# Performance work log

Measured on AMD Instinct MI355X. Metric: run time of the kernel, lower is better.

Reference implementation:

```python
import jax, jax.numpy as jnp
import numpy as np

NUM_CLUSTERS = 10
NUM_ITERS = 20
RTOL, ATOL = 1e-5, 1e-6  # torch.allclose defaults with atol=1e-6 as in source


def _kmeans(tokens, valid, key):
    """Weighted k-means equivalent to kmeans_fast over the valid subset.

    tokens: [n, d] float; valid: [n] bool. Invalid tokens get zero weight in the
    per-cluster means, which is mathematically identical to removing them
    (as the torch code does via boolean indexing) while keeping static shapes.
    """
    n, d = tokens.shape
    # init centroids = random choice of NUM_CLUSTERS valid tokens (torch uses randperm)
    r = jax.random.uniform(key, (n,))
    init_idx = jnp.argsort(jnp.where(valid, r, 2.0))[:NUM_CLUSTERS]
    centroids0 = tokens[init_idx]  # [K, d]
    w = valid.astype(tokens.dtype)  # [n]
    tok_sq = jnp.sum(tokens * tokens, axis=1)  # [n]

    def step(carry, _):
        c, done = carry
        # squared euclidean distances [n, K] via expansion (same math as sum((t-c)^2))
        d2 = tok_sq[:, None] - 2.0 * (tokens @ c.T) + jnp.sum(c * c, axis=1)[None, :]
        labels = jnp.argmin(d2, axis=1)  # [n]
        onehot = jax.nn.one_hot(labels, NUM_CLUSTERS, dtype=tokens.dtype) * w[:, None]
        counts = onehot.sum(axis=0)              # [K]
        sums = onehot.T @ tokens                 # [K, d]
        new_c = jnp.where(counts[:, None] > 0, sums / jnp.maximum(counts, 1.0)[:, None], c)
        conv = jnp.all(jnp.abs(c - new_c) <= ATOL + RTOL * jnp.abs(new_c))
        # torch breaks BEFORE assigning, so on convergence the OLD centroids are kept
        c_next = jnp.where(done | conv, c, new_c)
        return (c_next, done | conv), None

    (c, _), _ = jax.lax.scan(step, (centroids0, jnp.array(False)), None, length=NUM_ITERS)
    return c


def setup_inputs() -> dict:
    key = jax.random.key(0)
    kx, km = jax.random.split(key)
    x = jax.random.normal(kx, (1, 2048, 160, 160), dtype=jnp.float32)
    mask = jax.random.uniform(km, (1, 1, 160, 160), dtype=jnp.float32)
    return {"x": x, "mask": mask}


def reference(x, mask):
    # x: [1, C, H, W]; mask: [1, 1, H, W] (already matching spatial size)
    mb = (mask > 0).astype(mask.dtype)
    mb = jnp.transpose(mb, (1, 0, 2, 3))          # [1, 1, H, W]
    mask_emb = x * mb                              # [1, C, H, W]
    valid = jnp.any(mask_emb != 0, axis=(0, 1))    # [H, W]
    _, C, H, W = x.shape
    tokens = mask_emb[0].reshape(C, H * W).T       # [HW, C]
    valid = valid.reshape(-1)                      # [HW]
    # n_valid > 10 by construction -> kmeans branch (as in source for real masks)
    centroids = _kmeans(tokens, valid, jax.random.key(42))
    return centroids  # [10, C]
```

## Files before the change

### kernel.cpp

```cpp
#include <hip/hip_runtime.h>
#include <stdint.h>

#define HW 25600
#define C  2048
#define K  10
#define NITER 20
#define RTOL_ 1e-5f
#define ATOL_ 1e-6f
#define NCH 16
#define CCH (C / NCH)

__device__ __align__(4) unsigned char g_valid[HW];
__device__ __align__(4) unsigned char g_labels[HW];
__device__ float g_tok_sq[HW];
__device__ float g_r[HW];
__device__ __align__(16) float  g_cent[K * C];
__device__ __align__(16) double g_cent64[K * C];
__device__ float g_csq[K];
__device__ int   g_counts[K];
__device__ unsigned g_done;
__device__ double g_part[NCH * K * HW];
__device__ double g_spart[2 * K * C];
__device__ double g_psq[8 * HW];
__device__ __align__(4) unsigned char g_pany[8 * HW];

__global__ __launch_bounds__(256) void prepA_kernel(const float* __restrict__ X,
                                                    const float* __restrict__ mask) {
    const int chunk = blockIdx.x & 7;
    const int hw0 = (blockIdx.x >> 3) * 1024 + threadIdx.x * 4;
    const float4 m4 = *(const float4*)(mask + hw0);
    const float mb0 = (m4.x > 0.0f) ? 1.0f : 0.0f;
    const float mb1 = (m4.y > 0.0f) ? 1.0f : 0.0f;
    const float mb2 = (m4.z > 0.0f) ? 1.0f : 0.0f;
    const float mb3 = (m4.w > 0.0f) ? 1.0f : 0.0f;
    const float* xp = X + hw0 + (size_t)(chunk * 256) * HW;
    double a0 = 0.0, a1 = 0.0, a2 = 0.0, a3 = 0.0;
    int n0 = 0, n1 = 0, n2 = 0, n3 = 0;
    for (int cc = 0; cc < 256; ++cc) {
        const float4 x = *(const float4*)(xp + (size_t)cc * HW);
        float v0 = x.x * mb0, v1 = x.y * mb1, v2 = x.z * mb2, v3 = x.w * mb3;
        n0 |= (v0 != 0.0f); n1 |= (v1 != 0.0f);
        n2 |= (v2 != 0.0f); n3 |= (v3 != 0.0f);
        a0 = fma((double)v0, (double)v0, a0);
        a1 = fma((double)v1, (double)v1, a1);
        a2 = fma((double)v2, (double)v2, a2);
        a3 = fma((double)v3, (double)v3, a3);
    }
    double* ps = g_psq + chunk * HW + hw0;
    ps[0] = a0; ps[1] = a1; ps[2] = a2; ps[3] = a3;
    *(uchar4*)&g_pany[chunk * HW + hw0] =
        make_uchar4((unsigned char)n0, (unsigned char)n1,
                    (unsigned char)n2, (unsigned char)n3);
}

__device__ __forceinline__ uint32_t rotl32(uint32_t v, int d) {
    return (v << d) | (v >> (32 - d));
}

__global__ __launch_bounds__(256) void rng_kernel() {
    const int hw = blockIdx.x * 256 + threadIdx.x;
    double s0 = (g_psq[0 * HW + hw] + g_psq[1 * HW + hw]) +
                (g_psq[2 * HW + hw] + g_psq[3 * HW + hw]);
    double s1 = (g_psq[4 * HW + hw] + g_psq[5 * HW + hw]) +
                (g_psq[6 * HW + hw] + g_psq[7 * HW + hw]);
    g_tok_sq[hw] = (float)(s0 + s1);
    int any = 0;
#pragma unroll
    for (int j = 0; j < 8; ++j) any |= g_pany[j * HW + hw];
    g_valid[hw] = any ? 1 : 0;

    const uint32_t k0 = 0u, k1 = 42u;
    uint32_t ks[3] = {k0, k1, k0 ^ k1 ^ 0x1BD11BDAu};
    uint32_t x0 = 0u + ks[0];
    uint32_t x1 = (uint32_t)hw + ks[1];
    const int rot[2][4] = {{13, 15, 26, 6}, {17, 29, 16, 24}};
#pragma unroll
    for (int g = 0; g < 5; ++g) {
#pragma unroll
        for (int j = 0; j < 4; ++j) {
            x0 += x1;
            x1 = rotl32(x1, rot[g & 1][j]);
            x1 ^= x0;
        }
        x0 += ks[(g + 1) % 3];
        x1 += ks[(g + 2) % 3] + (uint32_t)(g + 1);
    }
    uint32_t bits = x0 ^ x1;
    float u = __uint_as_float((bits >> 9) | 0x3f800000u) - 1.0f;
    g_r[hw] = any ? u : 2.0f;
}

__global__ __launch_bounds__(1024) void select_kernel(const float* __restrict__ X,
                                                      const float* __restrict__ mask) {
    __shared__ unsigned long long wmin[16];
    __shared__ unsigned long long bcast;
    __shared__ int sh_idx[K];
    const int tid = threadIdx.x;
    const int lane = tid & 63, wv = tid >> 6;
    unsigned long long key[25];
#pragma unroll
    for (int j = 0; j < 25; ++j) {
        const int i = j * 1024 + tid;
        key[j] = ((unsigned long long)__float_as_uint(g_r[i]) << 32) | (unsigned)i;
    }
    for (int round = 0; round < K; ++round) {
        unsigned long long best = ~0ull;
#pragma unroll
        for (int j = 0; j < 25; ++j) best = (key[j] < best) ? key[j] : best;
#pragma unroll
        for (int off = 32; off > 0; off >>= 1) {
            unsigned long long o = __shfl_down(best, off, 64);
            best = (o < best) ? o : best;
        }
        if (lane == 0) wmin[wv] = best;
        __syncthreads();
        if (wv == 0) {
            unsigned long long b = (lane < 16) ? wmin[lane] : ~0ull;
#pragma unroll
            for (int off = 8; off > 0; off >>= 1) {
                unsigned long long o = __shfl_down(b, off, 64);
                b = (o < b) ? o : b;
            }
            if (lane == 0) { bcast = b; sh_idx[round] = (int)(b & 0xffffffffu); }
        }
        __syncthreads();
        const unsigned long long g = bcast;
#pragma unroll
        for (int j = 0; j < 25; ++j) if (key[j] == g) key[j] = ~0ull;
    }
    for (int e = tid; e < K * C; e += 1024) {
        int k = e >> 11, c = e & (C - 1);
        int id = sh_idx[k];
        float mb = (mask[id] > 0.0f) ? 1.0f : 0.0f;
        float v = X[(size_t)c * HW + id] * mb;
        g_cent[e] = v;
        g_cent64[e] = (double)v;
    }
    if (tid < K) g_counts[tid] = 0;
    if (tid == 0) g_done = 0u;
    __syncthreads();
    if (wv < K) {
        double a = 0.0;
        for (int c = lane; c < C; c += 64) {
            double v = (double)g_cent[wv * C + c];
            a = fma(v, v, a);
        }
#pragma unroll
        for (int off = 32; off > 0; off >>= 1) a += __shfl_down(a, off, 64);
        if (lane == 0) g_csq[wv] = (float)a;
    }
}

__global__ __launch_bounds__(256) void label1_kernel(const float* __restrict__ X) {
    if (g_done) return;
    const int chunk = blockIdx.x & (NCH - 1);
    const int hw0 = (blockIdx.x >> 4) * 512 + threadIdx.x * 2;
    const int c0 = chunk * CCH;
    const double* __restrict__ cp = g_cent64 + c0;
    double acc0[K], acc1[K];
#pragma unroll
    for (int k = 0; k < K; ++k) { acc0[k] = 0.0; acc1[k] = 0.0; }
    const float* xp = X + hw0 + (size_t)c0 * HW;
#pragma unroll 4
    for (int cc = 0; cc < CCH; ++cc) {
        const float2 x = *(const float2*)(xp + (size_t)cc * HW);
        const double x0 = (double)x.x, x1 = (double)x.y;
#pragma unroll
        for (int k = 0; k < K; ++k) {
            const double cv = cp[k * C + cc];
            acc0[k] = fma(x0, cv, acc0[k]);
            acc1[k] = fma(x1, cv, acc1[k]);
        }
    }
#pragma unroll
    for (int k = 0; k < K; ++k) {
        double2* pp = (double2*)(g_part + (chunk * K + k) * HW + hw0);
        *pp = make_double2(acc0[k], acc1[k]);
    }
}

__global__ __launch_bounds__(256) void label2_kernel() {
#pragma clang fp contract(off)
    if (g_done) return;
    __shared__ int shist[K];
    const int t = threadIdx.x;
    if (t < K) shist[t] = 0;
    __syncthreads();
    const int hw = blockIdx.x * 256 + t;
    const float tsq = g_tok_sq[hw];
    float best = INFINITY;
    int bl = 0;
#pragma unroll
    for (int k = 0; k < K; ++k) {
        double p[NCH];
#pragma unroll
        for (int j = 0; j < NCH; ++j) p[j] = g_part[(j * K + k) * HW + hw];
        double q0 = ((p[0] + p[1]) + (p[2] + p[3])) + ((p[4] + p[5]) + (p[6] + p[7]));
        double q1 = ((p[8] + p[9]) + (p[10] + p[11])) + ((p[12] + p[13]) + (p[14] + p[15]));
        double d = q0 + q1;
        float dotf = (float)d;
        float twod = 2.0f * dotf;
        float d2 = (tsq - twod) + g_csq[k];
        if (d2 < best) { best = d2; bl = k; }
    }
    const int valid = g_valid[hw];
    g_labels[hw] = valid ? (unsigned char)bl : (unsigned char)255;
    if (valid) atomicAdd(&shist[bl], 1);
    __syncthreads();
    if (t < K) atomicAdd(&g_counts[t], shist[t]);
}

__global__ __launch_bounds__(256) void sum_kernel(const float* __restrict__ X) {
    if (g_done) return;
    __shared__ double sacc[4][64 * 11];
    const int c = blockIdx.x >> 1;
    const int half = blockIdx.x & 1;
    const int wv = threadIdx.x >> 6, lane = threadIdx.x & 63;
    double* slots = &sacc[wv][lane * 11];
#pragma unroll
    for (int k = 0; k < 11; ++k) slots[k] = 0.0;
    const int base = half * (HW / 2) + wv * (HW / 8);
    const float4* xr = (const float4*)(X + (size_t)c * HW + base);
    const unsigned* lw = (const unsigned*)(g_labels + base);
    for (int t = 0; t < 13; ++t) {
        const int idx = t * 64 + lane;
        if (idx < 800) {
            const float4 x = xr[idx];
            const unsigned w = lw[idx];
            const int l0 = min((int)(w & 255u), 10);
            const int l1 = min((int)((w >> 8) & 255u), 10);
            const int l2 = min((int)((w >> 16) & 255u), 10);
            const int l3 = min((int)(w >> 24), 10);
            slots[l0] += (double)x.x;
            slots[l1] += (double)x.y;
            slots[l2] += (double)x.z;
            slots[l3] += (double)x.w;
        }
    }
    double acc[K];
#pragma unroll
    for (int k = 0; k < K; ++k) acc[k] = slots[k];
#pragma unroll
    for (int k = 0; k < K; ++k) {
#pragma unroll
        for (int off = 32; off > 0; off >>= 1) acc[k] += __shfl_down(acc[k], off, 64);
    }
    __shared__ double comb[4][K];
    if (lane == 0) {
#pragma unroll
        for (int k = 0; k < K; ++k) comb[wv][k] = acc[k];
    }
    __syncthreads();
    if (threadIdx.x < K) {
        const int k = threadIdx.x;
        double s = (comb[0][k] + comb[1][k]) + (comb[2][k] + comb[3][k]);
        g_spart[(half * K + k) * C + c] = s;
    }
}

__global__ __launch_bounds__(1024) void update_kernel(int last, float* __restrict__ out) {
#pragma clang fp contract(off)
    __shared__ float sh_counts[K];
    __shared__ int s_conv;
    __shared__ unsigned s_done;
    const int tid = threadIdx.x;
    if (tid == 0) { s_conv = 1; s_done = g_done; }
    if (tid < K) sh_counts[tid] = (float)g_counts[tid];
    __syncthreads();
    const bool dn = (s_done != 0);
    float newv[20], oldv[20];
    int convLocal = 1;
#pragma unroll
    for (int j = 0; j < 20; ++j) {
        int e = tid + j * 1024;
        int k = e >> 11;
        float cnt = sh_counts[k];
        float cv = g_cent[e];
        float sumf = (float)(g_spart[e] + g_spart[K * C + e]);
        float nv = (cnt > 0.0f) ? (sumf / fmaxf(cnt, 1.0f)) : cv;
        newv[j] = nv;
        oldv[j] = cv;
        float tol = RTOL_ * fabsf(nv);
        tol = ATOL_ + tol;
        float diff = fabsf(cv - nv);
        if (!(diff <= tol)) convLocal = 0;
    }
    if (!convLocal) atomicAnd(&s_conv, 0);
    __syncthreads();
    const bool conv = (s_conv != 0);
    const bool upd = (!dn && !conv);
#pragma unroll
    for (int j = 0; j < 20; ++j) {
        int e = tid + j * 1024;
        float fv = upd ? newv[j] : oldv[j];
        if (upd) { g_cent[e] = fv; g_cent64[e] = (double)fv; }
        if (last) out[e] = fv;
    }
    if (tid == 0 && conv && !dn) g_done = 1u;
    if (tid < K) g_counts[tid] = 0;
    __syncthreads();
    const int wv = tid >> 6, lane = tid & 63;
    if (wv < K) {
        double a = 0.0;
        for (int c = lane; c < C; c += 64) {
            double v = (double)g_cent[wv * C + c];
            a = fma(v, v, a);
        }
#pragma unroll
        for (int off = 32; off > 0; off >>= 1) a += __shfl_down(a, off, 64);
        if (lane == 0) g_csq[wv] = (float)a;
    }
}

extern "C" void kernel_launch(void* const* d_in, const int* in_sizes, int n_in,
                              void* d_out, int out_size, void* d_ws, size_t ws_size,
                              hipStream_t stream) {
    const float* X = (const float*)d_in[0];
    const float* mask = (const float*)d_in[1];
    float* out = (float*)d_out;
    (void)in_sizes; (void)n_in; (void)out_size; (void)d_ws; (void)ws_size;

    prepA_kernel<<<200, 256, 0, stream>>>(X, mask);
    rng_kernel<<<100, 256, 0, stream>>>();
    select_kernel<<<1, 1024, 0, stream>>>(X, mask);
    for (int it = 0; it < NITER; ++it) {
        label1_kernel<<<800, 256, 0, stream>>>(X);
        label2_kernel<<<100, 256, 0, stream>>>();
        sum_kernel<<<2 * C, 256, 0, stream>>>(X);
        update_kernel<<<1, 1024, 0, stream>>>(it == NITER - 1 ? 1 : 0, out);
    }
}
```

Measured before the change: 2.446 ms.

## Rebalance work split: fewer channel chunks, one hw per thread, single-pass sums

Label1 drops from 16 to 8 channel chunks, with each thread handling one spatial position instead of two. Grid size stays 800 blocks, and the partial-dot buffer and the reduction reads in label2 are halved. prepA moves from float4 per thread to scalar loads over 800 blocks. sum_kernel uses one block per channel over the full HW range instead of two halves, which removes the second partial sum. Per-thread channel loops get longer and per-thread ILP is lower, and the float4-to-scalar change may reduce load efficiency.

```diff
diff --git a/kernel.cpp b/kernel.cpp
--- a/kernel.cpp
+++ b/kernel.cpp
@@ -7,7 +7,7 @@
 #define NITER 20
 #define RTOL_ 1e-5f
 #define ATOL_ 1e-6f
-#define NCH 16
+#define NCH 8
 #define CCH (C / NCH)
 
 __device__ __align__(4) unsigned char g_valid[HW];
@@ -20,37 +20,25 @@
 __device__ int   g_counts[K];
 __device__ unsigned g_done;
 __device__ double g_part[NCH * K * HW];
-__device__ double g_spart[2 * K * C];
+__device__ double g_spart[K * C];
 __device__ double g_psq[8 * HW];
 __device__ __align__(4) unsigned char g_pany[8 * HW];
 
 __global__ __launch_bounds__(256) void prepA_kernel(const float* __restrict__ X,
                                                     const float* __restrict__ mask) {
     const int chunk = blockIdx.x & 7;
-    const int hw0 = (blockIdx.x >> 3) * 1024 + threadIdx.x * 4;
-    const float4 m4 = *(const float4*)(mask + hw0);
-    const float mb0 = (m4.x > 0.0f) ? 1.0f : 0.0f;
-    const float mb1 = (m4.y > 0.0f) ? 1.0f : 0.0f;
-    const float mb2 = (m4.z > 0.0f) ? 1.0f : 0.0f;
-    const float mb3 = (m4.w > 0.0f) ? 1.0f : 0.0f;
-    const float* xp = X + hw0 + (size_t)(chunk * 256) * HW;
-    double a0 = 0.0, a1 = 0.0, a2 = 0.0, a3 = 0.0;
-    int n0 = 0, n1 = 0, n2 = 0, n3 = 0;
+    const int hw = (blockIdx.x >> 3) * 256 + threadIdx.x;
+    const float mb = (mask[hw] > 0.0f) ? 1.0f : 0.0f;
+    const float* xp = X + hw + (size_t)(chunk * 256) * HW;
+    double a = 0.0;
+    int n = 0;
     for (int cc = 0; cc < 256; ++cc) {
-        const float4 x = *(const float4*)(xp + (size_t)cc * HW);
-        float v0 = x.x * mb0, v1 = x.y * mb1, v2 = x.z * mb2, v3 = x.w * mb3;
-        n0 |= (v0 != 0.0f); n1 |= (v1 != 0.0f);
-        n2 |= (v2 != 0.0f); n3 |= (v3 != 0.0f);
-        a0 = fma((double)v0, (double)v0, a0);
-        a1 = fma((double)v1, (double)v1, a1);
-        a2 = fma((double)v2, (double)v2, a2);
-        a3 = fma((double)v3, (double)v3, a3);
-    }
-    double* ps = g_psq + chunk * HW + hw0;
-    ps[0] = a0; ps[1] = a1; ps[2] = a2; ps[3] = a3;
-    *(uchar4*)&g_pany[chunk * HW + hw0] =
-        make_uchar4((unsigned char)n0, (unsigned char)n1,
-                    (unsigned char)n2, (unsigned char)n3);
+        float v = xp[(size_t)cc * HW] * mb;
+        n |= (v != 0.0f);
+        a = fma((double)v, (double)v, a);
+    }
+    g_psq[chunk * HW + hw] = a;
+    g_pany[chunk * HW + hw] = (unsigned char)n;
 }
 
 __device__ __forceinline__ uint32_t rotl32(uint32_t v, int d) {
@@ -154,29 +142,21 @@
 __global__ __launch_bounds__(256) void label1_kernel(const float* __restrict__ X) {
     if (g_done) return;
     const int chunk = blockIdx.x & (NCH - 1);
-    const int hw0 = (blockIdx.x >> 4) * 512 + threadIdx.x * 2;
+    const int hw = (blockIdx.x >> 3) * 256 + threadIdx.x;
     const int c0 = chunk * CCH;
     const double* __restrict__ cp = g_cent64 + c0;
-    double acc0[K], acc1[K];
-#pragma unroll
-    for (int k = 0; k < K; ++k) { acc0[k] = 0.0; acc1[k] = 0.0; }
-    const float* xp = X + hw0 + (size_t)c0 * HW;
+    double acc[K];
+#pragma unroll
+    for (int k = 0; k < K; ++k) acc[k] = 0.0;
+    const float* xp = X + hw + (size_t)c0 * HW;
 #pragma unroll 4
     for (int cc = 0; cc < CCH; ++cc) {
-        const float2 x = *(const float2*)(xp + (size_t)cc * HW);
-        const double x0 = (double)x.x, x1 = (double)x.y;
-#pragma unroll
-        for (int k = 0; k < K; ++k) {
-            const double cv = cp[k * C + cc];
-            acc0[k] = fma(x0, cv, acc0[k]);
-            acc1[k] = fma(x1, cv, acc1[k]);
-        }
-    }
-#pragma unroll
-    for (int k = 0; k < K; ++k) {
-        double2* pp = (double2*)(g_part + (chunk * K + k) * HW + hw0);
-        *pp = make_double2(acc0[k], acc1[k]);
-    }
+        const double x = (double)xp[(size_t)cc * HW];
+#pragma unroll
+        for (int k = 0; k < K; ++k) acc[k] = fma(x, cp[k * C + cc], acc[k]);
+    }
+#pragma unroll
+    for (int k = 0; k < K; ++k) g_part[(chunk * K + k) * HW + hw] = acc[k];
 }
 
 __global__ __launch_bounds__(256) void label2_kernel() {
@@ -195,9 +175,7 @@
         double p[NCH];
 #pragma unroll
         for (int j = 0; j < NCH; ++j) p[j] = g_part[(j * K + k) * HW + hw];
-        double q0 = ((p[0] + p[1]) + (p[2] + p[3])) + ((p[4] + p[5]) + (p[6] + p[7]));
-        double q1 = ((p[8] + p[9]) + (p[10] + p[11])) + ((p[12] + p[13]) + (p[14] + p[15]));
-        double d = q0 + q1;
+        double d = ((p[0] + p[1]) + (p[2] + p[3])) + ((p[4] + p[5]) + (p[6] + p[7]));
         float dotf = (float)d;
         float twod = 2.0f * dotf;
         float d2 = (tsq - twod) + g_csq[k];
@@ -213,29 +191,26 @@
 __global__ __launch_bounds__(256) void sum_kernel(const float* __restrict__ X) {
     if (g_done) return;
     __shared__ double sacc[4][64 * 11];
-    const int c = blockIdx.x >> 1;
-    const int half = blockIdx.x & 1;
+    const int c = blockIdx.x;
     const int wv = threadIdx.x >> 6, lane = threadIdx.x & 63;
     double* slots = &sacc[wv][lane * 11];
 #pragma unroll
     for (int k = 0; k < 11; ++k) slots[k] = 0.0;
-    const int base = half * (HW / 2) + wv * (HW / 8);
+    const int base = wv * (HW / 4);
     const float4* xr = (const float4*)(X + (size_t)c * HW + base);
     const unsigned* lw = (const unsigned*)(g_labels + base);
-    for (int t = 0; t < 13; ++t) {
+    for (int t = 0; t < 25; ++t) {
         const int idx = t * 64 + lane;
-        if (idx < 800) {
-            const float4 x = xr[idx];
-            const unsigned w = lw[idx];
-            const int l0 = min((int)(w & 255u), 10);
-            const int l1 = min((int)((w >> 8) & 255u), 10);
-            const int l2 = min((int)((w >> 16) & 255u), 10);
-            const int l3 = min((int)(w >> 24), 10);
-            slots[l0] += (double)x.x;
-            slots[l1] += (double)x.y;
-            slots[l2] += (double)x.z;
-            slots[l3] += (double)x.w;
-        }
+        const float4 x = xr[idx];
+        const unsigned w = lw[idx];
+        const int l0 = min((int)(w & 255u), 10);
+        const int l1 = min((int)((w >> 8) & 255u), 10);
+        const int l2 = min((int)((w >> 16) & 255u), 10);
+        const int l3 = min((int)(w >> 24), 10);
+        slots[l0] += (double)x.x;
+        slots[l1] += (double)x.y;
+        slots[l2] += (double)x.z;
+        slots[l3] += (double)x.w;
     }
     double acc[K];
 #pragma unroll
@@ -253,8 +228,7 @@
     __syncthreads();
     if (threadIdx.x < K) {
         const int k = threadIdx.x;
-        double s = (comb[0][k] + comb[1][k]) + (comb[2][k] + comb[3][k]);
-        g_spart[(half * K + k) * C + c] = s;
+        g_spart[k * C + c] = (comb[0][k] + comb[1][k]) + (comb[2][k] + comb[3][k]);
     }
 }
 
@@ -276,7 +250,7 @@
         int k = e >> 11;
         float cnt = sh_counts[k];
         float cv = g_cent[e];
-        float sumf = (float)(g_spart[e] + g_spart[K * C + e]);
+        float sumf = (float)g_spart[e];
         float nv = (cnt > 0.0f) ? (sumf / fmaxf(cnt, 1.0f)) : cv;
         newv[j] = nv;
         oldv[j] = cv;
@@ -320,13 +294,13 @@
     float* out = (float*)d_out;
     (void)in_sizes; (void)n_in; (void)out_size; (void)d_ws; (void)ws_size;
 
-    prepA_kernel<<<200, 256, 0, stream>>>(X, mask);
+    prepA_kernel<<<800, 256, 0, stream>>>(X, mask);
     rng_kernel<<<100, 256, 0, stream>>>();
     select_kernel<<<1, 1024, 0, stream>>>(X, mask);
     for (int it = 0; it < NITER; ++it) {
         label1_kernel<<<800, 256, 0, stream>>>(X);
         label2_kernel<<<100, 256, 0, stream>>>();
-        sum_kernel<<<2 * C, 256, 0, stream>>>(X);
+        sum_kernel<<<C, 256, 0, stream>>>(X);
         update_kernel<<<1, 1024, 0, stream>>>(it == NITER - 1 ? 1 : 0, out);
     }
 }
```

Measured after the change: 2.350 ms. 1.04x faster.
